# Optimization experiments

Hardware: AMD Instinct MI355X
Metric: run time of the kernel (lower is better)

The kernel has to match this reference:

```python
import jax, jax.numpy as jnp
import numpy as np

DIM = 384
HEADS = 6
HIDDEN = int(DIM * 4.0)
EPS = 1e-6

def setup_inputs() -> dict:
    key = jax.random.key(0)
    ks = jax.random.split(key, 8)
    s = 0.02
    return {
        "x": jax.random.normal(ks[0], (4, 2048, DIM), dtype=jnp.float32),
        "w_qkv": jax.random.normal(ks[1], (DIM, 3 * DIM), dtype=jnp.float32) * s,
        "b_qkv": jnp.zeros((3 * DIM,), dtype=jnp.float32),
        "w_proj": jax.random.normal(ks[2], (DIM, DIM), dtype=jnp.float32) * s,
        "b_proj": jnp.zeros((DIM,), dtype=jnp.float32),
        "w_fc1": jax.random.normal(ks[3], (DIM, HIDDEN), dtype=jnp.float32) * s,
        "b_fc1": jnp.zeros((HIDDEN,), dtype=jnp.float32),
        "w_fc2": jax.random.normal(ks[4], (HIDDEN, DIM), dtype=jnp.float32) * s,
        "b_fc2": jnp.zeros((DIM,), dtype=jnp.float32),
        "g1": jnp.ones((DIM,), dtype=jnp.float32),
        "beta1": jnp.zeros((DIM,), dtype=jnp.float32),
        "g2": jnp.ones((DIM,), dtype=jnp.float32),
        "beta2": jnp.zeros((DIM,), dtype=jnp.float32),
    }

def _layernorm(x, g, b):
    mu = jnp.mean(x, axis=-1, keepdims=True)
    var = jnp.mean(jnp.square(x - mu), axis=-1, keepdims=True)
    return (x - mu) * jax.lax.rsqrt(var + EPS) * g + b

def _attention(x, w_qkv, b_qkv, w_proj, b_proj):
    B, N, C = x.shape
    H = HEADS
    Dh = C // H
    qkv = x @ w_qkv + b_qkv                      # [B,N,3C]
    qkv = qkv.reshape(B, N, 3, H, Dh)
    q = jnp.transpose(qkv[:, :, 0], (0, 2, 1, 3))  # [B,H,N,Dh]
    k = jnp.transpose(qkv[:, :, 1], (0, 2, 1, 3))
    v = jnp.transpose(qkv[:, :, 2], (0, 2, 1, 3))
    scale = Dh ** -0.5
    attn = jnp.einsum('bhnd,bhmd->bhnm', q, k) * scale
    attn = jax.nn.softmax(attn, axis=-1)
    out = jnp.einsum('bhnm,bhmd->bhnd', attn, v)
    out = jnp.transpose(out, (0, 2, 1, 3)).reshape(B, N, C)
    return out @ w_proj + b_proj

def _mlp(x, w_fc1, b_fc1, w_fc2, b_fc2):
    h = jax.nn.gelu(x @ w_fc1 + b_fc1, approximate=False)
    return h @ w_fc2 + b_fc2

def reference(x, w_qkv, b_qkv, w_proj, b_proj, w_fc1, b_fc1, w_fc2, b_fc2, g1, beta1, g2, beta2):
    x = x + _attention(_layernorm(x, g1, beta1), w_qkv, b_qkv, w_proj, b_proj)
    x = x + _mlp(_layernorm(x, g2, beta2), w_fc1, b_fc1, w_fc2, b_fc2)
    return x
```

## Files before the change

kernel.cpp:

```cpp
#include <hip/hip_runtime.h>
#include <hip/hip_bf16.h>

#define TOK 8192
#define CDIM 384
#define HEADS 6
#define DH 64
#define HID 1536
#define SEQ 2048

#define QSCALE 0.18033688011112042f

typedef short bf16x8 __attribute__((ext_vector_type(8)));
typedef short bf16x4 __attribute__((ext_vector_type(4)));
typedef float f32x4 __attribute__((ext_vector_type(4)));
typedef float f32x16 __attribute__((ext_vector_type(16)));
typedef void __attribute__((address_space(1))) GV;
typedef void __attribute__((address_space(3))) SV;

__device__ __forceinline__ short f2bf(float f) {
    __hip_bfloat16 h = __float2bfloat16(f);
    return *reinterpret_cast<short*>(&h);
}

__device__ __forceinline__ int pack_bf2(float a, float b) {
    __hip_bfloat162 h2 = __float22bfloat162_rn(make_float2(a, b));
    int r;
    __builtin_memcpy(&r, &h2, 4);
    return r;
}

__device__ __forceinline__ void gl_lds16(const short* g, short* lds) {
    __builtin_amdgcn_global_load_lds((GV*)g, (SV*)lds, 16, 0, 0);
}

__device__ __forceinline__ float gelu_fast(float v) {
    const float A = 2.3022067f;
    const float B = 0.1029442f;
    const float u = v * (A + B * v * v);
    return v - v / (1.0f + exp2f(u));
}

__global__ __launch_bounds__(128) void ln_trans(const float* __restrict__ x,
                                                const float* __restrict__ g,
                                                const float* __restrict__ bta,
                                                short* __restrict__ y,
                                                const float* __restrict__ w_qkv,
                                                const float* __restrict__ w_proj,
                                                const float* __restrict__ w_fc1,
                                                const float* __restrict__ w_fc2,
                                                short* __restrict__ qkvT,
                                                short* __restrict__ projT,
                                                short* __restrict__ fc1T,
                                                short* __restrict__ fc2T) {
    if (blockIdx.x < TOK) {
        const int row = blockIdx.x;
        const float* xr = x + (size_t)row * CDIM;
        const int t = threadIdx.x;
        float v0 = xr[t], v1 = xr[t + 128], v2 = xr[t + 256];
        float s = v0 + v1 + v2;
        float ss = v0 * v0 + v1 * v1 + v2 * v2;
#pragma unroll
        for (int off = 1; off < 64; off <<= 1) {
            s += __shfl_xor(s, off);
            ss += __shfl_xor(ss, off);
        }
        __shared__ float sh[4];
        const int wv = t >> 6;
        if ((t & 63) == 0) { sh[wv] = s; sh[2 + wv] = ss; }
        __syncthreads();
        s = sh[0] + sh[1];
        ss = sh[2] + sh[3];
        const float mu = s * (1.0f / CDIM);
        const float var = ss * (1.0f / CDIM) - mu * mu;
        const float rs = rsqrtf(var + 1e-6f);
        short* yr = y + (size_t)row * CDIM;
        yr[t]       = f2bf((v0 - mu) * rs * g[t]       + bta[t]);
        yr[t + 128] = f2bf((v1 - mu) * rs * g[t + 128] + bta[t + 128]);
        yr[t + 256] = f2bf((v2 - mu) * rs * g[t + 256] + bta[t + 256]);
        return;
    }
    int b = blockIdx.x - TOK;
    const float* w; short* o; int K, N, nb;
    if (b < 432)       { w = w_qkv;  o = qkvT;  K = 384;  N = 1152; nb = 36; }
    else if (b < 576)  { b -= 432;  w = w_proj; o = projT; K = 384;  N = 384;  nb = 12; }
    else if (b < 1152) { b -= 576;  w = w_fc1;  o = fc1T;  K = 384;  N = 1536; nb = 48; }
    else               { b -= 1152; w = w_fc2;  o = fc2T;  K = 1536; N = 384;  nb = 12; }
    const int bx = (b % nb) * 32, by = (b / nb) * 32;
    __shared__ float t[32][33];
    const int tx = threadIdx.x & 31, ty = threadIdx.x >> 5;
#pragma unroll
    for (int i = 0; i < 8; ++i)
        t[ty + i * 4][tx] = w[(size_t)(by + ty + i * 4) * N + bx + tx];
    __syncthreads();
#pragma unroll
    for (int i = 0; i < 8; ++i)
        o[(size_t)(bx + ty + i * 4) * K + by + tx] = f2bf(t[tx][ty + i * 4]);
}

__global__ __launch_bounds__(128) void ln_kernel(const float* __restrict__ x,
                                                 const float* __restrict__ g,
                                                 const float* __restrict__ bta,
                                                 short* __restrict__ y) {
    const int row = blockIdx.x;
    const float* xr = x + (size_t)row * CDIM;
    const int t = threadIdx.x;
    float v0 = xr[t], v1 = xr[t + 128], v2 = xr[t + 256];
    float s = v0 + v1 + v2;
    float ss = v0 * v0 + v1 * v1 + v2 * v2;
#pragma unroll
    for (int off = 1; off < 64; off <<= 1) {
        s += __shfl_xor(s, off);
        ss += __shfl_xor(ss, off);
    }
    __shared__ float sh[4];
    const int wv = t >> 6;
    if ((t & 63) == 0) { sh[wv] = s; sh[2 + wv] = ss; }
    __syncthreads();
    s = sh[0] + sh[1];
    ss = sh[2] + sh[3];
    const float mu = s * (1.0f / CDIM);
    const float var = ss * (1.0f / CDIM) - mu * mu;
    const float rs = rsqrtf(var + 1e-6f);
    short* yr = y + (size_t)row * CDIM;
    yr[t]       = f2bf((v0 - mu) * rs * g[t]       + bta[t]);
    yr[t + 128] = f2bf((v1 - mu) * rs * g[t + 128] + bta[t + 128]);
    yr[t + 256] = f2bf((v2 - mu) * rs * g[t + 256] + bta[t + 256]);
}

template <int MODE, int MT>
__global__ __launch_bounds__(256) void mfma_gemm(const short* __restrict__ A,
                                                 const short* __restrict__ WT,
                                                 const float* __restrict__ bias,
                                                 const float* __restrict__ resid,
                                                 float* __restrict__ outF,
                                                 short* __restrict__ outB,
                                                 short* __restrict__ qb,
                                                 short* __restrict__ kb,
                                                 short* __restrict__ vtb,
                                                 int M, int N, int K) {
    constexpr int BN = (MT == 4) ? 128 : 64;
    constexpr int BM = (MT == 1) ? 64 : 128;
    __shared__ __align__(16) short As[BM * 64];
    __shared__ __align__(16) short Bs[BN * 64];

    const int tid  = threadIdx.x;
    const int w    = tid >> 6;
    const int lane = tid & 63;
    const int quad = lane >> 4;
    const int n15  = lane & 15;
    const int wr   = (MT == 4) ? (w >> 1) : w;
    const int wc   = (MT == 4) ? (w & 1) : 0;
    const int m0   = blockIdx.y * BM;
    const int n0   = blockIdx.x * BN;
    const int swz  = n15 & 7;

    f32x4 acc[MT][4];
#pragma unroll
    for (int i = 0; i < MT; ++i)
#pragma unroll
        for (int j = 0; j < 4; ++j) {
            acc[i][j][0] = 0; acc[i][j][1] = 0; acc[i][j][2] = 0; acc[i][j][3] = 0;
        }

    for (int k0 = 0; k0 < K; k0 += 64) {
        __syncthreads();
#pragma unroll
        for (int i = 0; i < BM / 32; ++i) {
            const int c = i * 256 + tid;
            const int r = c >> 3, p = c & 7;
            gl_lds16(A + (size_t)(m0 + r) * K + k0 + ((p ^ (r & 7)) * 8),
                     As + (i * 256 + w * 64) * 8);
        }
#pragma unroll
        for (int i = 0; i < BN / 32; ++i) {
            const int c = i * 256 + tid;
            const int r = c >> 3, p = c & 7;
            gl_lds16(WT + (size_t)(n0 + r) * K + k0 + ((p ^ (r & 7)) * 8),
                     Bs + (i * 256 + w * 64) * 8);
        }
        __syncthreads();

#pragma unroll
        for (int kk = 0; kk < 2; ++kk) {
            bf16x8 af[MT], bfr[4];
#pragma unroll
            for (int mt = 0; mt < MT; ++mt)
                af[mt] = *(const bf16x8*)&As[(wr * (MT * 16) + mt * 16 + n15) * 64 +
                                             (((kk * 4 + quad) ^ swz) * 8)];
#pragma unroll
            for (int nt = 0; nt < 4; ++nt)
                bfr[nt] = *(const bf16x8*)&Bs[(wc * 64 + nt * 16 + n15) * 64 +
                                              (((kk * 4 + quad) ^ swz) * 8)];
#pragma unroll
            for (int mt = 0; mt < MT; ++mt)
#pragma unroll
                for (int nt = 0; nt < 4; ++nt)
                    acc[mt][nt] = __builtin_amdgcn_mfma_f32_16x16x32_bf16(af[mt], bfr[nt], acc[mt][nt], 0, 0, 0);
        }
    }

#pragma unroll
    for (int nt = 0; nt < 4; ++nt) {
        const int col = n0 + wc * 64 + nt * 16 + n15;
        const float bv = bias[col];
        if constexpr (MODE == 2) {
            const int part = col / CDIM;
            const int rem  = col - part * CDIM;
            const int h    = rem >> 6;
            const int d    = rem & 63;
#pragma unroll
            for (int mt = 0; mt < MT; ++mt) {
                const int r0 = m0 + wr * (MT * 16) + mt * 16 + quad * 4;
                const int bi = r0 >> 11;
                const int n  = r0 & 2047;
                if (part == 2) {
                    short4 pkv;
                    pkv.x = f2bf(acc[mt][nt][0] + bv);
                    pkv.y = f2bf(acc[mt][nt][1] + bv);
                    pkv.z = f2bf(acc[mt][nt][2] + bv);
                    pkv.w = f2bf(acc[mt][nt][3] + bv);
                    *(short4*)&vtb[((size_t)(bi * HEADS + h) * DH + d) * SEQ + n] = pkv;
                } else {
                    short* dst = (part == 0 ? qb : kb) +
                                 ((size_t)(bi * HEADS + h) * SEQ + n) * DH + d;
#pragma unroll
                    for (int rr = 0; rr < 4; ++rr) {
                        float o = acc[mt][nt][rr] + bv;
                        if (part == 0) o *= QSCALE;
                        dst[(size_t)rr * DH] = f2bf(o);
                    }
                }
            }
        } else {
#pragma unroll
            for (int mt = 0; mt < MT; ++mt)
#pragma unroll
                for (int rr = 0; rr < 4; ++rr) {
                    const int r = m0 + wr * (MT * 16) + mt * 16 + quad * 4 + rr;
                    float o = acc[mt][nt][rr] + bv;
                    if constexpr (MODE == 1) {
                        outB[(size_t)r * N + col] = f2bf(gelu_fast(o));
                    } else {
                        if (resid) o += resid[(size_t)r * N + col];
                        outF[(size_t)r * N + col] = o;
                    }
                }
        }
    }
}

__global__ __launch_bounds__(256, 4) void attn_mfma(const short* __restrict__ qb,
                                                    const short* __restrict__ kb,
                                                    const short* __restrict__ vtb,
                                                    short* __restrict__ outp) {
    __shared__ __align__(16) char smem[33792];

    const int bid = blockIdx.x;
    const int x   = bid & 7;
    const int j   = bid >> 3;
    const int bh  = x * 3 + (j >> 6);
    const int qt  = j & 63;
    const int bi  = bh / HEADS;
    const int h   = bh - bi * HEADS;

    const int tid  = threadIdx.x;
    const int w    = tid >> 6;
    const int lane = tid & 63;
    const int l31  = lane & 31;
    const int hi   = lane >> 5;

    short* Kl  = (short*)(smem + w * 8192);
    short* Vtl = (short*)(smem + w * 8192 + 4096);

    const size_t headoff = (size_t)bh * SEQ * DH;

    bf16x8 qf[4];
    {
        const short* qg = qb + headoff + (size_t)(qt * 32 + l31) * DH + hi * 8;
#pragma unroll
        for (int kc = 0; kc < 4; ++kc)
            qf[kc] = *(const bf16x8*)(qg + kc * 16);
    }
    asm volatile("s_waitcnt vmcnt(0)" ::: "memory");

    const int l3 = lane >> 3, l7 = lane & 7;
    const int l2 = lane >> 2, p4 = lane & 3;
    const short* kg = kb + headoff + (size_t)(w * 32 + l3) * DH + ((l7 ^ l3) * 8);
    const short* vg = vtb + (size_t)bh * DH * SEQ + (size_t)l2 * SEQ +
                      ((p4 ^ (l2 & 3)) * 8) + w * 32;

    const int swk = l31 & 7;
    const int swv = l31 & 3;
    const int krd = l31 * 64;
    const int vrd = l31 * 32;

    f32x16 O0 = {}, O1 = {}, Lc = {};
    const f32x16 Zc = {};

    bf16x8 ones;
    {
        const short one = 0x3F80;
#pragma unroll
        for (int i = 0; i < 8; ++i) ones[i] = one;
    }

#define STAGE_K(tt) { const short* kgt = kg + (size_t)(tt) * 128 * DH;             \
        _Pragma("unroll") for (int i = 0; i < 4; ++i)                              \
            gl_lds16(kgt + i * 512, Kl + i * 512); }
#define STAGE_V(tt) { const short* vgt = vg + (tt) * 128;                          \
        _Pragma("unroll") for (int i = 0; i < 4; ++i)                              \
            gl_lds16(vgt + (size_t)i * 16 * SEQ, Vtl + i * 512); }

    STAGE_K(0);
    STAGE_V(0);

    for (int t = 0; t < SEQ / 128; ++t) {
        asm volatile("s_waitcnt vmcnt(4)" ::: "memory");
        __builtin_amdgcn_sched_barrier(0);

        bf16x8 kf0 = *(const bf16x8*)&Kl[krd + (((0 + hi) ^ swk) * 8)];
        bf16x8 kf1 = *(const bf16x8*)&Kl[krd + (((2 + hi) ^ swk) * 8)];
        bf16x8 kf2 = *(const bf16x8*)&Kl[krd + (((4 + hi) ^ swk) * 8)];
        bf16x8 kf3 = *(const bf16x8*)&Kl[krd + (((6 + hi) ^ swk) * 8)];
        asm volatile("s_waitcnt lgkmcnt(0)" ::: "memory");
        __builtin_amdgcn_sched_barrier(0);
        if (t < SEQ / 128 - 1) STAGE_K(t + 1);

        f32x16 S = __builtin_amdgcn_mfma_f32_32x32x16_bf16(kf0, qf[0], Zc, 0, 0, 0);
        S = __builtin_amdgcn_mfma_f32_32x32x16_bf16(kf1, qf[1], S, 0, 0, 0);
        S = __builtin_amdgcn_mfma_f32_32x32x16_bf16(kf2, qf[2], S, 0, 0, 0);
        S = __builtin_amdgcn_mfma_f32_32x32x16_bf16(kf3, qf[3], S, 0, 0, 0);

        if (t < SEQ / 128 - 1) {
            asm volatile("s_waitcnt vmcnt(4)" ::: "memory");
        } else {
            asm volatile("s_waitcnt vmcnt(0)" ::: "memory");
        }
        __builtin_amdgcn_sched_barrier(0);

        bf16x8 v00 = *(const bf16x8*)&Vtl[vrd + ((hi ^ swv) * 8)];
        bf16x8 v01 = *(const bf16x8*)&Vtl[vrd + (((2 + hi) ^ swv) * 8)];
        bf16x8 v10 = *(const bf16x8*)&Vtl[1024 + vrd + ((hi ^ swv) * 8)];
        bf16x8 v11 = *(const bf16x8*)&Vtl[1024 + vrd + (((2 + hi) ^ swv) * 8)];
        asm volatile("s_waitcnt lgkmcnt(0)" ::: "memory");
        __builtin_amdgcn_sched_barrier(0);
        if (t < SEQ / 128 - 1) STAGE_V(t + 1);

        float e[16];
#pragma unroll
        for (int r = 0; r < 16; ++r) e[r] = exp2f(S[r]);

        int p0 = pack_bf2(e[0], e[1]),  p1 = pack_bf2(e[2], e[3]);
        int p2 = pack_bf2(e[4], e[5]),  p3 = pack_bf2(e[6], e[7]);
        asm("v_permlane32_swap_b32 %0, %1" : "+v"(p0), "+v"(p2));
        asm("v_permlane32_swap_b32 %0, %1" : "+v"(p1), "+v"(p3));
        int p4w = pack_bf2(e[8], e[9]),  p5 = pack_bf2(e[10], e[11]);
        int p6 = pack_bf2(e[12], e[13]), p7 = pack_bf2(e[14], e[15]);
        asm("v_permlane32_swap_b32 %0, %1" : "+v"(p4w), "+v"(p6));
        asm("v_permlane32_swap_b32 %0, %1" : "+v"(p5), "+v"(p7));
        bf16x8 pf0, pf1;
        { int pw[4] = {p0, p1, p2, p3};   __builtin_memcpy(&pf0, pw, 16); }
        { int pw[4] = {p4w, p5, p6, p7};  __builtin_memcpy(&pf1, pw, 16); }

        O0 = __builtin_amdgcn_mfma_f32_32x32x16_bf16(v00, pf0, O0, 0, 0, 0);
        O0 = __builtin_amdgcn_mfma_f32_32x32x16_bf16(v01, pf1, O0, 0, 0, 0);
        O1 = __builtin_amdgcn_mfma_f32_32x32x16_bf16(v10, pf0, O1, 0, 0, 0);
        O1 = __builtin_amdgcn_mfma_f32_32x32x16_bf16(v11, pf1, O1, 0, 0, 0);
        Lc = __builtin_amdgcn_mfma_f32_32x32x16_bf16(ones, pf0, Lc, 0, 0, 0);
        Lc = __builtin_amdgcn_mfma_f32_32x32x16_bf16(ones, pf1, Lc, 0, 0, 0);
    }
#undef STAGE_K
#undef STAGE_V

    __syncthreads();
    float* Obuf = (float*)smem;
    float* lbuf = (float*)(smem + 33280);
    float* myO  = Obuf + w * 2080;
#pragma unroll
    for (int r = 0; r < 16; ++r) {
        const int d0 = (r & 3) + 8 * (r >> 2) + 4 * hi;
        myO[l31 * 65 + d0]      = O0[r];
        myO[l31 * 65 + 32 + d0] = O1[r];
    }
    if (hi == 0) lbuf[w * 32 + l31] = Lc[0];
    __syncthreads();

    const int quad = lane >> 4;
    const int n15  = lane & 15;
    const int d = w * 16 + n15;
#pragma unroll
    for (int i = 0; i < 8; ++i) {
        const int q = quad * 8 + i;
        const float l = lbuf[q] + lbuf[32 + q] + lbuf[64 + q] + lbuf[96 + q];
        const float s = Obuf[q * 65 + d] + Obuf[2080 + q * 65 + d] +
                        Obuf[4160 + q * 65 + d] + Obuf[6240 + q * 65 + d];
        outp[(size_t)(bi * SEQ + qt * 32 + q) * CDIM + h * DH + d] = f2bf(s / l);
    }
}

extern "C" void kernel_launch(void* const* d_in, const int* in_sizes, int n_in,
                              void* d_out, int out_size, void* d_ws, size_t ws_size,
                              hipStream_t stream) {
    const float* x      = (const float*)d_in[0];
    const float* w_qkv  = (const float*)d_in[1];
    const float* b_qkv  = (const float*)d_in[2];
    const float* w_proj = (const float*)d_in[3];
    const float* b_proj = (const float*)d_in[4];
    const float* w_fc1  = (const float*)d_in[5];
    const float* b_fc1  = (const float*)d_in[6];
    const float* w_fc2  = (const float*)d_in[7];
    const float* b_fc2  = (const float*)d_in[8];
    const float* g1     = (const float*)d_in[9];
    const float* beta1  = (const float*)d_in[10];
    const float* g2     = (const float*)d_in[11];
    const float* beta2  = (const float*)d_in[12];
    float* out = (float*)d_out;

    short* qkvT = (short*)d_ws;
    short* projT = qkvT + 1152 * 384;
    short* fc1T  = projT + 384 * 384;
    short* fc2T  = fc1T + 1536 * 384;
    short* y     = fc2T + 384 * 1536;
    short* qb    = y + (size_t)TOK * 384;
    short* kb    = qb + (size_t)TOK * 384;
    short* vtb   = kb + (size_t)TOK * 384;
    short* attn  = vtb + (size_t)TOK * 384;
    short* hbuf  = attn + (size_t)TOK * 384;

    ln_trans<<<TOK + 1728, 128, 0, stream>>>(x, g1, beta1, y,
                                             w_qkv, w_proj, w_fc1, w_fc2,
                                             qkvT, projT, fc1T, fc2T);
    mfma_gemm<2, 4><<<dim3(1152 / 128, TOK / 128), 256, 0, stream>>>(
        y, qkvT, b_qkv, nullptr, nullptr, nullptr, qb, kb, vtb, TOK, 3 * CDIM, CDIM);
    attn_mfma<<<1536, 256, 0, stream>>>(qb, kb, vtb, attn);
    mfma_gemm<0, 1><<<dim3(CDIM / 64, TOK / 64), 256, 0, stream>>>(
        attn, projT, b_proj, x, out, nullptr, nullptr, nullptr, nullptr, TOK, CDIM, CDIM);
    ln_kernel<<<TOK, 128, 0, stream>>>(out, g2, beta2, y);
    mfma_gemm<1, 4><<<dim3(HID / 128, TOK / 128), 256, 0, stream>>>(
        y, fc1T, b_fc1, nullptr, nullptr, hbuf, nullptr, nullptr, nullptr, TOK, HID, CDIM);
    mfma_gemm<0, 1><<<dim3(CDIM / 64, TOK / 64), 256, 0, stream>>>(
        hbuf, fc2T, b_fc2, out, out, nullptr, nullptr, nullptr, nullptr, TOK, CDIM, HID);
}
```

Measured before the change: 235.0 us.

## Double-buffer small-tile GEMM and use hardware exp2 and packed bf16 convert

For the MT==1 GEMM variant, K-tiles are now double-buffered in LDS so the global-to-LDS load of the next tile overlaps the MFMA work on the current one, with one barrier per step. Separately, exp2f calls in GELU and the attention softmax become the raw hardware exp2 builtin, and the bf16 packing helper becomes a single v_cvt_pk_bf16_f32 instruction. The aim is to hide load latency in the proj/fc2 GEMMs and cut ALU instructions in the attention inner loop. The costs are doubled LDS use for that variant and losing exp2f's denormal/range handling.

```diff
diff --git a/kernel.cpp b/kernel.cpp
--- a/kernel.cpp
+++ b/kernel.cpp
@@ -17,15 +17,20 @@
 typedef void __attribute__((address_space(1))) GV;
 typedef void __attribute__((address_space(3))) SV;
 
+#if __has_builtin(__builtin_amdgcn_exp2f)
+#define EXP2(x) __builtin_amdgcn_exp2f(x)
+#else
+#define EXP2(x) exp2f(x)
+#endif
+
 __device__ __forceinline__ short f2bf(float f) {
     __hip_bfloat16 h = __float2bfloat16(f);
     return *reinterpret_cast<short*>(&h);
 }
 
-__device__ __forceinline__ int pack_bf2(float a, float b) {
-    __hip_bfloat162 h2 = __float22bfloat162_rn(make_float2(a, b));
+__device__ __forceinline__ int cvt_pk_bf16(float lo, float hi) {
     int r;
-    __builtin_memcpy(&r, &h2, 4);
+    asm("v_cvt_pk_bf16_f32 %0, %1, %2" : "=v"(r) : "v"(lo), "v"(hi));
     return r;
 }
 
@@ -37,7 +42,7 @@
     const float A = 2.3022067f;
     const float B = 0.1029442f;
     const float u = v * (A + B * v * v);
-    return v - v / (1.0f + exp2f(u));
+    return v - v / (1.0f + EXP2(u));
 }
 
 __global__ __launch_bounds__(128) void ln_trans(const float* __restrict__ x,
@@ -140,8 +145,9 @@
                                                  int M, int N, int K) {
     constexpr int BN = (MT == 4) ? 128 : 64;
     constexpr int BM = (MT == 1) ? 64 : 128;
-    __shared__ __align__(16) short As[BM * 64];
-    __shared__ __align__(16) short Bs[BN * 64];
+    constexpr int BUFS = (MT == 1) ? 2 : 1;
+    __shared__ __align__(16) short As[BUFS * BM * 64];
+    __shared__ __align__(16) short Bs[BUFS * BN * 64];
 
     const int tid  = threadIdx.x;
     const int w    = tid >> 6;
@@ -162,40 +168,96 @@
             acc[i][j][0] = 0; acc[i][j][1] = 0; acc[i][j][2] = 0; acc[i][j][3] = 0;
         }
 
-    for (int k0 = 0; k0 < K; k0 += 64) {
-        __syncthreads();
-#pragma unroll
-        for (int i = 0; i < BM / 32; ++i) {
-            const int c = i * 256 + tid;
-            const int r = c >> 3, p = c & 7;
-            gl_lds16(A + (size_t)(m0 + r) * K + k0 + ((p ^ (r & 7)) * 8),
-                     As + (i * 256 + w * 64) * 8);
+    if constexpr (MT == 1) {
+        const int nk = K >> 6;
+#define STAGE1(buf, k0)                                                        \
+    {                                                                          \
+        short* Ad = As + (buf) * 4096;                                         \
+        short* Bd = Bs + (buf) * 4096;                                         \
+        _Pragma("unroll")                                                      \
+        for (int i = 0; i < 2; ++i) {                                          \
+            const int c = i * 256 + tid;                                       \
+            const int r = c >> 3, p = c & 7;                                   \
+            gl_lds16(A + (size_t)(m0 + r) * K + (k0) + ((p ^ (r & 7)) * 8),    \
+                     Ad + (i * 256 + w * 64) * 8);                             \
+        }                                                                      \
+        _Pragma("unroll")                                                      \
+        for (int i = 0; i < 2; ++i) {                                          \
+            const int c = i * 256 + tid;                                       \
+            const int r = c >> 3, p = c & 7;                                   \
+            gl_lds16(WT + (size_t)(n0 + r) * K + (k0) + ((p ^ (r & 7)) * 8),   \
+                     Bd + (i * 256 + w * 64) * 8);                             \
+        }                                                                      \
+    }
+#define COMPUTE1(buf)                                                          \
+    {                                                                          \
+        const short* Ab = As + (buf) * 4096;                                   \
+        const short* Bb = Bs + (buf) * 4096;                                   \
+        _Pragma("unroll")                                                      \
+        for (int kk = 0; kk < 2; ++kk) {                                       \
+            bf16x8 af = *(const bf16x8*)&Ab[(w * 16 + n15) * 64 +              \
+                                            (((kk * 4 + quad) ^ swz) * 8)];    \
+            bf16x8 bfr[4];                                                     \
+            _Pragma("unroll")                                                  \
+            for (int nt = 0; nt < 4; ++nt)                                     \
+                bfr[nt] = *(const bf16x8*)&Bb[(nt * 16 + n15) * 64 +           \
+                                              (((kk * 4 + quad) ^ swz) * 8)];  \
+            _Pragma("unroll")                                                  \
+            for (int nt = 0; nt < 4; ++nt)                                     \
+                acc[0][nt] = __builtin_amdgcn_mfma_f32_16x16x32_bf16(          \
+                    af, bfr[nt], acc[0][nt], 0, 0, 0);                         \
+        }                                                                      \
+    }
+        STAGE1(0, 0);
+        asm volatile("s_waitcnt vmcnt(0)" ::: "memory");
+        __builtin_amdgcn_s_barrier();
+        int cur = 0;
+        for (int ks = 0; ks < nk - 1; ++ks) {
+            STAGE1(cur ^ 1, (ks + 1) << 6);
+            COMPUTE1(cur);
+            asm volatile("s_waitcnt vmcnt(0)" ::: "memory");
+            __builtin_amdgcn_s_barrier();
+            cur ^= 1;
         }
-#pragma unroll
-        for (int i = 0; i < BN / 32; ++i) {
-            const int c = i * 256 + tid;
-            const int r = c >> 3, p = c & 7;
-            gl_lds16(WT + (size_t)(n0 + r) * K + k0 + ((p ^ (r & 7)) * 8),
-                     Bs + (i * 256 + w * 64) * 8);
-        }
-        __syncthreads();
-
-#pragma unroll
-        for (int kk = 0; kk < 2; ++kk) {
-            bf16x8 af[MT], bfr[4];
-#pragma unroll
-            for (int mt = 0; mt < MT; ++mt)
-                af[mt] = *(const bf16x8*)&As[(wr * (MT * 16) + mt * 16 + n15) * 64 +
-                                             (((kk * 4 + quad) ^ swz) * 8)];
-#pragma unroll
-            for (int nt = 0; nt < 4; ++nt)
-                bfr[nt] = *(const bf16x8*)&Bs[(wc * 64 + nt * 16 + n15) * 64 +
-                                              (((kk * 4 + quad) ^ swz) * 8)];
-#pragma unroll
-            for (int mt = 0; mt < MT; ++mt)
+        COMPUTE1(cur);
+#undef STAGE1
+#undef COMPUTE1
+    } else {
+        for (int k0 = 0; k0 < K; k0 += 64) {
+            __syncthreads();
+#pragma unroll
+            for (int i = 0; i < BM / 32; ++i) {
+                const int c = i * 256 + tid;
+                const int r = c >> 3, p = c & 7;
+                gl_lds16(A + (size_t)(m0 + r) * K + k0 + ((p ^ (r & 7)) * 8),
+                         As + (i * 256 + w * 64) * 8);
+            }
+#pragma unroll
+            for (int i = 0; i < BN / 32; ++i) {
+                const int c = i * 256 + tid;
+                const int r = c >> 3, p = c & 7;
+                gl_lds16(WT + (size_t)(n0 + r) * K + k0 + ((p ^ (r & 7)) * 8),
+                         Bs + (i * 256 + w * 64) * 8);
+            }
+            __syncthreads();
+
+#pragma unroll
+            for (int kk = 0; kk < 2; ++kk) {
+                bf16x8 af[MT], bfr[4];
+#pragma unroll
+                for (int mt = 0; mt < MT; ++mt)
+                    af[mt] = *(const bf16x8*)&As[(wr * (MT * 16) + mt * 16 + n15) * 64 +
+                                                 (((kk * 4 + quad) ^ swz) * 8)];
 #pragma unroll
                 for (int nt = 0; nt < 4; ++nt)
-                    acc[mt][nt] = __builtin_amdgcn_mfma_f32_16x16x32_bf16(af[mt], bfr[nt], acc[mt][nt], 0, 0, 0);
+                    bfr[nt] = *(const bf16x8*)&Bs[(wc * 64 + nt * 16 + n15) * 64 +
+                                                  (((kk * 4 + quad) ^ swz) * 8)];
+#pragma unroll
+                for (int mt = 0; mt < MT; ++mt)
+#pragma unroll
+                    for (int nt = 0; nt < 4; ++nt)
+                        acc[mt][nt] = __builtin_amdgcn_mfma_f32_16x16x32_bf16(af[mt], bfr[nt], acc[mt][nt], 0, 0, 0);
+            }
         }
     }
 
@@ -348,14 +410,14 @@
 
         float e[16];
 #pragma unroll
-        for (int r = 0; r < 16; ++r) e[r] = exp2f(S[r]);
-
-        int p0 = pack_bf2(e[0], e[1]),  p1 = pack_bf2(e[2], e[3]);
-        int p2 = pack_bf2(e[4], e[5]),  p3 = pack_bf2(e[6], e[7]);
+        for (int r = 0; r < 16; ++r) e[r] = EXP2(S[r]);
+
+        int p0 = cvt_pk_bf16(e[0], e[1]),   p1 = cvt_pk_bf16(e[2], e[3]);
+        int p2 = cvt_pk_bf16(e[4], e[5]),   p3 = cvt_pk_bf16(e[6], e[7]);
         asm("v_permlane32_swap_b32 %0, %1" : "+v"(p0), "+v"(p2));
         asm("v_permlane32_swap_b32 %0, %1" : "+v"(p1), "+v"(p3));
-        int p4w = pack_bf2(e[8], e[9]),  p5 = pack_bf2(e[10], e[11]);
-        int p6 = pack_bf2(e[12], e[13]), p7 = pack_bf2(e[14], e[15]);
+        int p4w = cvt_pk_bf16(e[8], e[9]),  p5 = cvt_pk_bf16(e[10], e[11]);
+        int p6 = cvt_pk_bf16(e[12], e[13]), p7 = cvt_pk_bf16(e[14], e[15]);
         asm("v_permlane32_swap_b32 %0, %1" : "+v"(p4w), "+v"(p6));
         asm("v_permlane32_swap_b32 %0, %1" : "+v"(p5), "+v"(p7));
         bf16x8 pf0, pf1;
```

Result: faster. 227.2 us (-3.3%).
